# Optimization experiments

Measured on AMD Instinct MI355X. Metric: run time of the kernel, lower is better.

The kernel has to match this reference:

```python
import jax, jax.numpy as jnp
import numpy as np

N, E = 32768, 8192            # num_nodes, num_hyperedges
ND, ED, HD, OD, NH = 128, 128, 64, 128, 4  # node/edge/hidden/output dims, heads
EPS = 1e-8


def min_max_normalize(x):
    # per-feature (column-wise) min-max normalization, as in utils.min_max_normalize_cuda
    mn = x.min(axis=0)
    mx = x.max(axis=0)
    return (x - mn) / (mx - mn + EPS)


def setup_inputs() -> dict:
    key = jax.random.key(0)
    ks = jax.random.split(key, 12)
    s = 0.05
    node_features = jax.random.normal(ks[0], (N, ND), jnp.float32)
    # sparse-ish binary incidence matrix stored dense (as the torch code uses dense mm)
    incidence_matrix = (jax.random.uniform(ks[1], (N, E)) < 0.01).astype(jnp.float32)
    edge_features = jax.random.normal(ks[2], (E, ED), jnp.float32)
    # stacked per-head parameters (heads are chained, so head input dim == ND == OD)
    nodeW = jax.random.normal(ks[3], (NH, ND, HD), jnp.float32) * s
    nodeB = jnp.zeros((NH, HD), jnp.float32)
    edgeW = jax.random.normal(ks[4], (NH, ED, HD), jnp.float32) * s
    edgeB = jnp.zeros((NH, HD), jnp.float32)
    attnW = jax.random.normal(ks[5], (NH, HD, 1), jnp.float32) * s
    attnB = jnp.zeros((NH, 1), jnp.float32)
    outW = jax.random.normal(ks[6], (NH, HD, OD), jnp.float32) * s
    outB = jnp.zeros((NH, OD), jnp.float32)
    return dict(node_features=node_features, incidence_matrix=incidence_matrix,
                edge_features=edge_features, nodeW=nodeW, nodeB=nodeB,
                edgeW=edgeW, edgeB=edgeB, attnW=attnW, attnB=attnB,
                outW=outW, outB=outB)


def reference(node_features, incidence_matrix, edge_features,
              nodeW, nodeB, edgeW, edgeB, attnW, attnB, outW, outB):
    # node degree normalizer, shared across heads
    deg = incidence_matrix.sum(axis=1, keepdims=True) + EPS  # [N, 1]
    x = node_features
    for h in range(NH):  # heads are applied sequentially (chained), per original forward
        tn = x @ nodeW[h] + nodeB[h]                       # [N, HD]
        te = edge_features @ edgeW[h] + edgeB[h]           # [E, HD]
        agg = (incidence_matrix @ te) / deg                # [N, HD] mean over incident edges
        scores = (tn + agg) @ attnW[h] + attnB[h]          # [N, 1]
        scores = jnp.where(scores >= 0, scores, 0.2 * scores)  # LeakyReLU(0.2)
        coeffs = jax.nn.sigmoid(scores)                    # [N, 1]
        upd = coeffs * agg + tn                            # gated residual
        upd = upd @ outW[h] + outB[h]                      # [N, OD]
        upd = min_max_normalize(upd)
        x = jax.nn.relu(upd)                               # ReLU applied after each head
    # dropout is identity at inference; output_transform is defined but never used
    return x
```

## Files before the change

### kernel.cpp

```cpp
#include <hip/hip_runtime.h>
#include <cstdint>
#include <cstddef>

#define N_NODES 32768
#define N_EDGES 8192
#define ND 128
#define HD 64
#define OD 128
#define NH 4
#define EPSV 1e-8f

#define WPB 4
#define CAP 512
#define LCAP 16

__device__ __forceinline__ unsigned encf(float f) {
  unsigned b = __float_as_uint(f);
  return (b & 0x80000000u) ? ~b : (b | 0x80000000u);
}
__device__ __forceinline__ float decf(unsigned u) {
  unsigned b = (u & 0x80000000u) ? (u & 0x7fffffffu) : ~u;
  return __uint_as_float(b);
}

__global__ __launch_bounds__(256) void k_prep(
    const float* __restrict__ inc, const float* __restrict__ ef,
    float* __restrict__ P, float* __restrict__ deg)
{
  __shared__ int s_seg[WPB][64][LCAP];
  __shared__ __align__(16) int s_dense[WPB][CAP];
  const int t = threadIdx.x;
  const int lane = t & 63;
  const int wv = t >> 6;
  const int node = blockIdx.x * WPB + wv;
  const float* row = inc + (size_t)node * N_EDGES + lane * 4;

  float4 r[8];
  #pragma unroll
  for (int i = 0; i < 8; i++) r[i] = *(const float4*)(row + i * 256);
  int c = 0;
  #pragma unroll
  for (int o = 0; o < 4; o++) {
    #pragma unroll
    for (int i = 0; i < 8; i++) {
      const float4 v = r[i];
      const int nx = (o + 1) * 8 + i;
      if (nx < 32) r[i] = *(const float4*)(row + nx * 256);
      const int col0 = (o * 8 + i) * 256 + lane * 4;
      if (v.x != 0.f) { s_seg[wv][lane][c & (LCAP - 1)] = col0 + 0; c++; }
      if (v.y != 0.f) { s_seg[wv][lane][c & (LCAP - 1)] = col0 + 1; c++; }
      if (v.z != 0.f) { s_seg[wv][lane][c & (LCAP - 1)] = col0 + 2; c++; }
      if (v.w != 0.f) { s_seg[wv][lane][c & (LCAP - 1)] = col0 + 3; c++; }
    }
  }

  int pre = c;
  #pragma unroll
  for (int o = 1; o < 64; o <<= 1) {
    const int tv = __shfl_up(pre, o, 64);
    if (lane >= o) pre += tv;
  }
  const int total0 = __shfl(pre, 63, 64);
  const int excl = pre - c;
  if (lane == 0) deg[node] = (float)total0 + EPSV;

  const int cc = (c < LCAP) ? c : LCAP;
  for (int i = 0; i < cc; i++) {
    const int p = excl + i;
    if (p < CAP) s_dense[wv][p] = s_seg[wv][lane][i];
  }
  const int total = (total0 < CAP) ? total0 : CAP;

  const float* efl = ef + lane;
  float acc0 = 0.f, acc1 = 0.f;
  int i = 0;
  for (; i + 4 <= total; i += 4) {
    const int4 cs = *(const int4*)&s_dense[wv][i];
    const float a0 = efl[(size_t)cs.x * ND], b0 = efl[(size_t)cs.x * ND + 64];
    const float a1 = efl[(size_t)cs.y * ND], b1 = efl[(size_t)cs.y * ND + 64];
    const float a2 = efl[(size_t)cs.z * ND], b2 = efl[(size_t)cs.z * ND + 64];
    const float a3 = efl[(size_t)cs.w * ND], b3 = efl[(size_t)cs.w * ND + 64];
    acc0 += (a0 + a1) + (a2 + a3);
    acc1 += (b0 + b1) + (b2 + b3);
  }
  for (; i < total; i++) {
    const int cx = s_dense[wv][i];
    acc0 += efl[(size_t)cx * ND];
    acc1 += efl[(size_t)cx * ND + 64];
  }
  P[(size_t)node * ND + lane] = acc0;
  P[(size_t)node * ND + 64 + lane] = acc1;
}

__global__ __launch_bounds__(512, 4) void k_head(
    const float* __restrict__ xin, const float* __restrict__ P,
    const float* __restrict__ deg,
    const float* __restrict__ nodeW, const float* __restrict__ nodeB,
    const float* __restrict__ edgeW, const float* __restrict__ edgeB,
    const float* __restrict__ attnW, const float* __restrict__ attnB,
    const float* __restrict__ outW, const float* __restrict__ outB,
    const unsigned* __restrict__ pmn, const unsigned* __restrict__ pmx,
    unsigned* __restrict__ omn, unsigned* __restrict__ omx,
    float* __restrict__ y, const int do_norm)
{
  constexpr int LDW = 129;
  __shared__ float xs[64 * LDW];
  __shared__ float ps[64 * LDW];
  __shared__ float s_att[8 * 64];
  __shared__ float s_mm[2 * 4 * 128];
  const int t = threadIdx.x;
  const int r0 = blockIdx.x * 64;
  const int lane = t & 63;
  const int wv = __builtin_amdgcn_readfirstlane(t >> 6);

  #pragma unroll
  for (int i = 0; i < 4; i++) {
    const int f = t + i * 512;
    const int row = f >> 5;
    const int c4 = (f & 31) * 4;
    float4 xv = *(const float4*)(xin + (size_t)(r0 + row) * ND + c4);
    const float4 pv = *(const float4*)(P + (size_t)(r0 + row) * ND + c4);
    float xa[4] = {xv.x, xv.y, xv.z, xv.w};
    if (do_norm) {
      #pragma unroll
      for (int c = 0; c < 4; c++) {
        const float mn = decf(pmn[c4 + c]);
        const float mx = decf(pmx[c4 + c]);
        const float v = (xa[c] - mn) / (mx - mn + EPSV);
        xa[c] = v > 0.f ? v : 0.f;
      }
    }
    const float pa[4] = {pv.x, pv.y, pv.z, pv.w};
    #pragma unroll
    for (int c = 0; c < 4; c++) {
      xs[row * LDW + c4 + c] = xa[c];
      ps[row * LDW + c4 + c] = pa[c];
    }
  }
  __syncthreads();

  const int j0 = wv * 8;
  float tn[8], agg[8];
  #pragma unroll
  for (int j = 0; j < 8; j++) { tn[j] = 0.f; agg[j] = 0.f; }
  const float* xrow = &xs[lane * LDW];
  const float* prow = &ps[lane * LDW];
  #pragma unroll 4
  for (int k = 0; k < ND; k++) {
    const float xv = xrow[k];
    const float pv = prow[k];
    const float* nw = nodeW + (size_t)k * HD + j0;
    const float* ew = edgeW + (size_t)k * HD + j0;
    #pragma unroll
    for (int j = 0; j < 8; j++) {
      tn[j] = fmaf(xv, nw[j], tn[j]);
      agg[j] = fmaf(pv, ew[j], agg[j]);
    }
  }

  const float d = deg[r0 + lane];
  const float rsum = d - EPSV;
  const float inv_d = 1.f / d;
  float sp = 0.f;
  #pragma unroll
  for (int j = 0; j < 8; j++) {
    const float tj = tn[j] + nodeB[j0 + j];
    const float aj = fmaf(rsum, edgeB[j0 + j], agg[j]) * inv_d;
    tn[j] = tj;
    agg[j] = aj;
    sp = fmaf(tj + aj, attnW[j0 + j], sp);
  }
  s_att[wv * 64 + lane] = sp;
  __syncthreads();
  float s = attnB[0];
  #pragma unroll
  for (int w = 0; w < 8; w++) s += s_att[w * 64 + lane];
  s = (s >= 0.f) ? s : 0.2f * s;
  const float coeff = 1.f / (1.f + expf(-s));

  float* us = ps;
  #pragma unroll
  for (int j = 0; j < 8; j++) {
    us[lane * 65 + j0 + j] = fmaf(coeff, agg[j], tn[j]);
  }
  __syncthreads();

  const int jo0 = wv * 16;
  float yacc[16];
  #pragma unroll
  for (int i = 0; i < 16; i++) yacc[i] = outB[jo0 + i];
  #pragma unroll 4
  for (int k = 0; k < HD; k++) {
    const float uv = us[lane * 65 + k];
    const float* ow = outW + (size_t)k * OD + jo0;
    #pragma unroll
    for (int i = 0; i < 16; i++) yacc[i] = fmaf(uv, ow[i], yacc[i]);
  }

  float* ys = xs;
  #pragma unroll
  for (int i = 0; i < 16; i++) ys[lane * LDW + jo0 + i] = yacc[i];
  __syncthreads();
  #pragma unroll
  for (int i = 0; i < 4; i++) {
    const int f = t + i * 512;
    const int row = f >> 5;
    const int c4 = (f & 31) * 4;
    const float4 o = make_float4(ys[row * LDW + c4 + 0], ys[row * LDW + c4 + 1],
                                 ys[row * LDW + c4 + 2], ys[row * LDW + c4 + 3]);
    *(float4*)(y + (size_t)(r0 + row) * OD + c4) = o;
  }
  const int col = t & 127;
  const int sub = t >> 7;
  float lo = 3.4e38f, hi = -3.4e38f;
  for (int r = sub; r < 64; r += 4) {
    const float v = ys[r * LDW + col];
    lo = fminf(lo, v);
    hi = fmaxf(hi, v);
  }
  s_mm[sub * 128 + col] = lo;
  s_mm[512 + sub * 128 + col] = hi;
  __syncthreads();
  if (t < 128) {
    float l = s_mm[col];
    float h2 = s_mm[512 + col];
    #pragma unroll
    for (int ss = 1; ss < 4; ss++) {
      l = fminf(l, s_mm[ss * 128 + col]);
      h2 = fmaxf(h2, s_mm[512 + ss * 128 + col]);
    }
    atomicMin(&omn[col], encf(l));
    atomicMax(&omx[col], encf(h2));
  }
}

__global__ __launch_bounds__(256) void k_final(
    const float* __restrict__ y, const unsigned* __restrict__ mn_enc,
    const unsigned* __restrict__ mx_enc, float* __restrict__ out)
{
  const int i = blockIdx.x * 256 + threadIdx.x;
  const int col = i & (OD - 1);
  const float mn = decf(mn_enc[col]);
  const float mx = decf(mx_enc[col]);
  const float v = (y[i] - mn) / (mx - mn + EPSV);
  out[i] = (v > 0.f) ? v : 0.f;
}

extern "C" void kernel_launch(void* const* d_in, const int* in_sizes, int n_in,
                              void* d_out, int out_size, void* d_ws, size_t ws_size,
                              hipStream_t stream)
{
  const float* node_features = (const float*)d_in[0];
  const float* incidence     = (const float*)d_in[1];
  const float* edge_features = (const float*)d_in[2];
  const float* nodeW = (const float*)d_in[3];
  const float* nodeB = (const float*)d_in[4];
  const float* edgeW = (const float*)d_in[5];
  const float* edgeB = (const float*)d_in[6];
  const float* attnW = (const float*)d_in[7];
  const float* attnB = (const float*)d_in[8];
  const float* outW  = (const float*)d_in[9];
  const float* outB  = (const float*)d_in[10];
  float* out = (float*)d_out;

  float* P   = (float*)d_ws;
  float* yA  = P + (size_t)N_NODES * ND;
  float* yB  = yA + (size_t)N_NODES * OD;
  float* deg = yB + (size_t)N_NODES * OD;
  unsigned* mn = (unsigned*)(deg + N_NODES);
  unsigned* mx = mn + NH * OD;

  hipMemsetAsync(mn, 0xFF, NH * OD * sizeof(unsigned), stream);
  hipMemsetAsync(mx, 0x00, NH * OD * sizeof(unsigned), stream);

  k_prep<<<N_NODES / WPB, 256, 0, stream>>>(incidence, edge_features, P, deg);

  float* ybuf[2] = {yA, yB};
  for (int h = 0; h < NH; h++) {
    const float* xin = (h == 0) ? node_features : ybuf[(h + 1) & 1];
    float* yout = ybuf[h & 1];
    const unsigned* pmn = (h == 0) ? mn : mn + (size_t)(h - 1) * OD;
    const unsigned* pmx = (h == 0) ? mx : mx + (size_t)(h - 1) * OD;
    k_head<<<N_NODES / 64, 512, 0, stream>>>(
        xin, P, deg,
        nodeW + (size_t)h * ND * HD, nodeB + (size_t)h * HD,
        edgeW + (size_t)h * ND * HD, edgeB + (size_t)h * HD,
        attnW + (size_t)h * HD, attnB + h,
        outW + (size_t)h * HD * OD, outB + (size_t)h * OD,
        pmn, pmx, mn + (size_t)h * OD, mx + (size_t)h * OD,
        yout, (h > 0) ? 1 : 0);
  }
  k_final<<<(N_NODES * OD) / 256, 256, 0, stream>>>(
      ybuf[(NH - 1) & 1], mn + (size_t)(NH - 1) * OD, mx + (size_t)(NH - 1) * OD, out);
}
```

Measured before the change: 1.585 ms.

## Fuse all attention heads and final normalization into one cooperative kernel

Replaces the four per-head launches and the final normalization kernel with a single cooperative kernel. Each block keeps its 64 node rows resident in LDS across heads and uses grid-wide syncs to exchange the per-column min/max. This removes the intermediate y buffer round trips through global memory and the extra launch overheads. It requires all 512 blocks to be co-resident, so the launch depends on per-CU occupancy (LDS and registers) and adds grid barrier costs.

```diff
diff --git a/kernel.cpp b/kernel.cpp
--- a/kernel.cpp
+++ b/kernel.cpp
@@ -1,6 +1,9 @@
 #include <hip/hip_runtime.h>
+#include <hip/hip_cooperative_groups.h>
 #include <cstdint>
 #include <cstddef>
+
+namespace cg = cooperative_groups;
 
 #define N_NODES 32768
 #define N_EDGES 8192
@@ -92,158 +95,174 @@
   P[(size_t)node * ND + 64 + lane] = acc1;
 }
 
-__global__ __launch_bounds__(512, 4) void k_head(
-    const float* __restrict__ xin, const float* __restrict__ P,
+__global__ __launch_bounds__(512, 4) void k_fused(
+    const float* __restrict__ x0, const float* __restrict__ P,
     const float* __restrict__ deg,
     const float* __restrict__ nodeW, const float* __restrict__ nodeB,
     const float* __restrict__ edgeW, const float* __restrict__ edgeB,
     const float* __restrict__ attnW, const float* __restrict__ attnB,
     const float* __restrict__ outW, const float* __restrict__ outB,
-    const unsigned* __restrict__ pmn, const unsigned* __restrict__ pmx,
-    unsigned* __restrict__ omn, unsigned* __restrict__ omx,
-    float* __restrict__ y, const int do_norm)
+    unsigned* __restrict__ mnb, unsigned* __restrict__ mxb,
+    float* __restrict__ out)
 {
   constexpr int LDW = 129;
   __shared__ float xs[64 * LDW];
   __shared__ float ps[64 * LDW];
-  __shared__ float s_att[8 * 64];
-  __shared__ float s_mm[2 * 4 * 128];
+  float* const usT   = xs;
+  float* const s_att = xs + 4096;
+  cg::grid_group grid = cg::this_grid();
+
   const int t = threadIdx.x;
   const int r0 = blockIdx.x * 64;
   const int lane = t & 63;
   const int wv = __builtin_amdgcn_readfirstlane(t >> 6);
+  const int j0 = wv * 8;
+  const int jo0 = wv * 16;
 
   #pragma unroll
   for (int i = 0; i < 4; i++) {
     const int f = t + i * 512;
     const int row = f >> 5;
     const int c4 = (f & 31) * 4;
-    float4 xv = *(const float4*)(xin + (size_t)(r0 + row) * ND + c4);
+    const float4 xv = *(const float4*)(x0 + (size_t)(r0 + row) * ND + c4);
     const float4 pv = *(const float4*)(P + (size_t)(r0 + row) * ND + c4);
-    float xa[4] = {xv.x, xv.y, xv.z, xv.w};
-    if (do_norm) {
-      #pragma unroll
-      for (int c = 0; c < 4; c++) {
-        const float mn = decf(pmn[c4 + c]);
-        const float mx = decf(pmx[c4 + c]);
-        const float v = (xa[c] - mn) / (mx - mn + EPSV);
-        xa[c] = v > 0.f ? v : 0.f;
-      }
-    }
-    const float pa[4] = {pv.x, pv.y, pv.z, pv.w};
-    #pragma unroll
-    for (int c = 0; c < 4; c++) {
-      xs[row * LDW + c4 + c] = xa[c];
-      ps[row * LDW + c4 + c] = pa[c];
-    }
-  }
-  __syncthreads();
-
-  const int j0 = wv * 8;
-  float tn[8], agg[8];
-  #pragma unroll
-  for (int j = 0; j < 8; j++) { tn[j] = 0.f; agg[j] = 0.f; }
-  const float* xrow = &xs[lane * LDW];
-  const float* prow = &ps[lane * LDW];
-  #pragma unroll 4
-  for (int k = 0; k < ND; k++) {
-    const float xv = xrow[k];
-    const float pv = prow[k];
-    const float* nw = nodeW + (size_t)k * HD + j0;
-    const float* ew = edgeW + (size_t)k * HD + j0;
-    #pragma unroll
-    for (int j = 0; j < 8; j++) {
-      tn[j] = fmaf(xv, nw[j], tn[j]);
-      agg[j] = fmaf(pv, ew[j], agg[j]);
-    }
-  }
-
+    xs[row * LDW + c4 + 0] = xv.x; xs[row * LDW + c4 + 1] = xv.y;
+    xs[row * LDW + c4 + 2] = xv.z; xs[row * LDW + c4 + 3] = xv.w;
+    ps[row * LDW + c4 + 0] = pv.x; ps[row * LDW + c4 + 1] = pv.y;
+    ps[row * LDW + c4 + 2] = pv.z; ps[row * LDW + c4 + 3] = pv.w;
+  }
   const float d = deg[r0 + lane];
   const float rsum = d - EPSV;
   const float inv_d = 1.f / d;
-  float sp = 0.f;
-  #pragma unroll
-  for (int j = 0; j < 8; j++) {
-    const float tj = tn[j] + nodeB[j0 + j];
-    const float aj = fmaf(rsum, edgeB[j0 + j], agg[j]) * inv_d;
-    tn[j] = tj;
-    agg[j] = aj;
-    sp = fmaf(tj + aj, attnW[j0 + j], sp);
-  }
-  s_att[wv * 64 + lane] = sp;
   __syncthreads();
-  float s = attnB[0];
-  #pragma unroll
-  for (int w = 0; w < 8; w++) s += s_att[w * 64 + lane];
-  s = (s >= 0.f) ? s : 0.2f * s;
-  const float coeff = 1.f / (1.f + expf(-s));
-
-  float* us = ps;
-  #pragma unroll
-  for (int j = 0; j < 8; j++) {
-    us[lane * 65 + j0 + j] = fmaf(coeff, agg[j], tn[j]);
-  }
-  __syncthreads();
-
-  const int jo0 = wv * 16;
-  float yacc[16];
-  #pragma unroll
-  for (int i = 0; i < 16; i++) yacc[i] = outB[jo0 + i];
-  #pragma unroll 4
-  for (int k = 0; k < HD; k++) {
-    const float uv = us[lane * 65 + k];
-    const float* ow = outW + (size_t)k * OD + jo0;
-    #pragma unroll
-    for (int i = 0; i < 16; i++) yacc[i] = fmaf(uv, ow[i], yacc[i]);
-  }
-
-  float* ys = xs;
-  #pragma unroll
-  for (int i = 0; i < 16; i++) ys[lane * LDW + jo0 + i] = yacc[i];
-  __syncthreads();
-  #pragma unroll
-  for (int i = 0; i < 4; i++) {
-    const int f = t + i * 512;
-    const int row = f >> 5;
-    const int c4 = (f & 31) * 4;
-    const float4 o = make_float4(ys[row * LDW + c4 + 0], ys[row * LDW + c4 + 1],
-                                 ys[row * LDW + c4 + 2], ys[row * LDW + c4 + 3]);
-    *(float4*)(y + (size_t)(r0 + row) * OD + c4) = o;
-  }
-  const int col = t & 127;
-  const int sub = t >> 7;
-  float lo = 3.4e38f, hi = -3.4e38f;
-  for (int r = sub; r < 64; r += 4) {
-    const float v = ys[r * LDW + col];
-    lo = fminf(lo, v);
-    hi = fmaxf(hi, v);
-  }
-  s_mm[sub * 128 + col] = lo;
-  s_mm[512 + sub * 128 + col] = hi;
-  __syncthreads();
-  if (t < 128) {
-    float l = s_mm[col];
-    float h2 = s_mm[512 + col];
-    #pragma unroll
-    for (int ss = 1; ss < 4; ss++) {
-      l = fminf(l, s_mm[ss * 128 + col]);
-      h2 = fmaxf(h2, s_mm[512 + ss * 128 + col]);
-    }
-    atomicMin(&omn[col], encf(l));
-    atomicMax(&omx[col], encf(h2));
-  }
-}
-
-__global__ __launch_bounds__(256) void k_final(
-    const float* __restrict__ y, const unsigned* __restrict__ mn_enc,
-    const unsigned* __restrict__ mx_enc, float* __restrict__ out)
-{
-  const int i = blockIdx.x * 256 + threadIdx.x;
-  const int col = i & (OD - 1);
-  const float mn = decf(mn_enc[col]);
-  const float mx = decf(mx_enc[col]);
-  const float v = (y[i] - mn) / (mx - mn + EPSV);
-  out[i] = (v > 0.f) ? v : 0.f;
+
+  for (int h = 0; h < NH; ++h) {
+    const float* nW = nodeW + (size_t)h * ND * HD;
+    const float* nB = nodeB + (size_t)h * HD;
+    const float* eW = edgeW + (size_t)h * ND * HD;
+    const float* eB = edgeB + (size_t)h * HD;
+    const float* aW = attnW + (size_t)h * HD;
+    const float* aB = attnB + h;
+    const float* oW = outW + (size_t)h * HD * OD;
+    const float* oB = outB + (size_t)h * OD;
+
+    float tn[8], agg[8];
+    #pragma unroll
+    for (int j = 0; j < 8; j++) { tn[j] = 0.f; agg[j] = 0.f; }
+    const float* xrow = &xs[lane * LDW];
+    const float* prow = &ps[lane * LDW];
+    #pragma unroll 4
+    for (int k = 0; k < ND; k++) {
+      const float xv = xrow[k];
+      const float pv = prow[k];
+      const float* nw = nW + (size_t)k * HD + j0;
+      const float* ew = eW + (size_t)k * HD + j0;
+      #pragma unroll
+      for (int j = 0; j < 8; j++) {
+        tn[j] = fmaf(xv, nw[j], tn[j]);
+        agg[j] = fmaf(pv, ew[j], agg[j]);
+      }
+    }
+
+    float sp = 0.f;
+    #pragma unroll
+    for (int j = 0; j < 8; j++) {
+      const float tj = tn[j] + nB[j0 + j];
+      const float aj = fmaf(rsum, eB[j0 + j], agg[j]) * inv_d;
+      tn[j] = tj;
+      agg[j] = aj;
+      sp = fmaf(tj + aj, aW[j0 + j], sp);
+    }
+    __syncthreads();
+    s_att[wv * 64 + lane] = sp;
+    __syncthreads();
+    float s = aB[0];
+    #pragma unroll
+    for (int w = 0; w < 8; w++) s += s_att[w * 64 + lane];
+    s = (s >= 0.f) ? s : 0.2f * s;
+    const float coeff = 1.f / (1.f + expf(-s));
+
+    #pragma unroll
+    for (int j = 0; j < 8; j++) {
+      usT[(j0 + j) * 64 + lane] = fmaf(coeff, agg[j], tn[j]);
+    }
+    __syncthreads();
+
+    float yacc[16];
+    #pragma unroll
+    for (int i = 0; i < 16; i++) yacc[i] = oB[jo0 + i];
+    #pragma unroll 4
+    for (int k = 0; k < HD; k++) {
+      const float uv = usT[k * 64 + lane];
+      const float* ow = oW + (size_t)k * OD + jo0;
+      #pragma unroll
+      for (int i = 0; i < 16; i++) yacc[i] = fmaf(uv, ow[i], yacc[i]);
+    }
+    __syncthreads();
+
+    #pragma unroll
+    for (int i = 0; i < 16; i++) xs[lane * LDW + jo0 + i] = yacc[i];
+    __syncthreads();
+
+    const int col = jo0 + (lane & 15);
+    const int rg = lane >> 4;
+    float lo = 3.4e38f, hi = -3.4e38f;
+    #pragma unroll 4
+    for (int i = 0; i < 16; i++) {
+      const float v = xs[(rg + 4 * i) * LDW + col];
+      lo = fminf(lo, v);
+      hi = fmaxf(hi, v);
+    }
+    lo = fminf(lo, __shfl_xor(lo, 16, 64));
+    hi = fmaxf(hi, __shfl_xor(hi, 16, 64));
+    lo = fminf(lo, __shfl_xor(lo, 32, 64));
+    hi = fmaxf(hi, __shfl_xor(hi, 32, 64));
+    if (rg == 0) {
+      atomicMin(&mnb[h * OD + col], encf(lo));
+      atomicMax(&mxb[h * OD + col], encf(hi));
+    }
+    __threadfence();
+    grid.sync();
+
+    if (h < NH - 1) {
+      #pragma unroll
+      for (int i = 0; i < 4; i++) {
+        const int f = t + i * 512;
+        const int row = f >> 5;
+        const int c4 = (f & 31) * 4;
+        #pragma unroll
+        for (int c = 0; c < 4; c++) {
+          const float mn = decf(__hip_atomic_load(&mnb[h * OD + c4 + c],
+                                __ATOMIC_RELAXED, __HIP_MEMORY_SCOPE_AGENT));
+          const float mx = decf(__hip_atomic_load(&mxb[h * OD + c4 + c],
+                                __ATOMIC_RELAXED, __HIP_MEMORY_SCOPE_AGENT));
+          const int idx = row * LDW + c4 + c;
+          const float v = (xs[idx] - mn) / (mx - mn + EPSV);
+          xs[idx] = (v > 0.f) ? v : 0.f;
+        }
+      }
+      __syncthreads();
+    } else {
+      #pragma unroll
+      for (int i = 0; i < 4; i++) {
+        const int f = t + i * 512;
+        const int row = f >> 5;
+        const int c4 = (f & 31) * 4;
+        float o[4];
+        #pragma unroll
+        for (int c = 0; c < 4; c++) {
+          const float mn = decf(__hip_atomic_load(&mnb[h * OD + c4 + c],
+                                __ATOMIC_RELAXED, __HIP_MEMORY_SCOPE_AGENT));
+          const float mx = decf(__hip_atomic_load(&mxb[h * OD + c4 + c],
+                                __ATOMIC_RELAXED, __HIP_MEMORY_SCOPE_AGENT));
+          const float v = (xs[row * LDW + c4 + c] - mn) / (mx - mn + EPSV);
+          o[c] = (v > 0.f) ? v : 0.f;
+        }
+        *(float4*)(out + (size_t)(r0 + row) * OD + c4) =
+            make_float4(o[0], o[1], o[2], o[3]);
+      }
+    }
+  }
 }
 
 extern "C" void kernel_launch(void* const* d_in, const int* in_sizes, int n_in,
@@ -264,9 +283,7 @@
   float* out = (float*)d_out;
 
   float* P   = (float*)d_ws;
-  float* yA  = P + (size_t)N_NODES * ND;
-  float* yB  = yA + (size_t)N_NODES * OD;
-  float* deg = yB + (size_t)N_NODES * OD;
+  float* deg = P + (size_t)N_NODES * ND;
   unsigned* mn = (unsigned*)(deg + N_NODES);
   unsigned* mx = mn + NH * OD;
 
@@ -275,21 +292,11 @@
 
   k_prep<<<N_NODES / WPB, 256, 0, stream>>>(incidence, edge_features, P, deg);
 
-  float* ybuf[2] = {yA, yB};
-  for (int h = 0; h < NH; h++) {
-    const float* xin = (h == 0) ? node_features : ybuf[(h + 1) & 1];
-    float* yout = ybuf[h & 1];
-    const unsigned* pmn = (h == 0) ? mn : mn + (size_t)(h - 1) * OD;
-    const unsigned* pmx = (h == 0) ? mx : mx + (size_t)(h - 1) * OD;
-    k_head<<<N_NODES / 64, 512, 0, stream>>>(
-        xin, P, deg,
-        nodeW + (size_t)h * ND * HD, nodeB + (size_t)h * HD,
-        edgeW + (size_t)h * ND * HD, edgeB + (size_t)h * HD,
-        attnW + (size_t)h * HD, attnB + h,
-        outW + (size_t)h * HD * OD, outB + (size_t)h * OD,
-        pmn, pmx, mn + (size_t)h * OD, mx + (size_t)h * OD,
-        yout, (h > 0) ? 1 : 0);
-  }
-  k_final<<<(N_NODES * OD) / 256, 256, 0, stream>>>(
-      ybuf[(NH - 1) & 1], mn + (size_t)(NH - 1) * OD, mx + (size_t)(NH - 1) * OD, out);
-}
+  void* args[] = {
+      (void*)&node_features, (void*)&P, (void*)&deg,
+      (void*)&nodeW, (void*)&nodeB, (void*)&edgeW, (void*)&edgeB,
+      (void*)&attnW, (void*)&attnB, (void*)&outW, (void*)&outB,
+      (void*)&mn, (void*)&mx, (void*)&out};
+  hipLaunchCooperativeKernel((void*)k_fused, dim3(N_NODES / 64), dim3(512),
+                             args, 0, stream);
+}
```

New measurement: 2.036 ms. 28.5% more time.
